# Optimization experiments

Hardware: AMD Instinct MI355X
Metric: run time of the kernel (lower is better)

Reference implementation:

```python
import jax, jax.numpy as jnp
import numpy as np
from jax import lax

B, DIM, H, W = 4, 128, 256, 256
SD, FD, GD = DIM // 2, DIM // 4, DIM // 4
EPS = 1e-6


def conv1x1(x, w):
    # w: (O, I), x: (B, I, H, W)
    return jnp.einsum('oi,bihw->bohw', w, x)


def dwconv3(x, w):
    # depthwise 3x3, w: (C, 1, 3, 3)
    return lax.conv_general_dilated(
        x, w, window_strides=(1, 1), padding='SAME',
        feature_group_count=x.shape[1],
        dimension_numbers=('NCHW', 'OIHW', 'NCHW'))


def rmsnorm(x, scale):
    rms = jnp.sqrt(jnp.mean(x * x, axis=1, keepdims=True) + EPS)
    return x / rms * scale[None, :, None, None]


def setup_inputs() -> dict:
    key = jax.random.key(0)
    ks = jax.random.split(key, 12)
    s = 0.02
    return {
        'x': jax.random.normal(ks[0], (B, DIM, H, W), jnp.float32),
        'norm1_scale': jnp.ones((DIM,), jnp.float32),
        'wq': jax.random.normal(ks[1], (SD, SD), jnp.float32) * s,
        'wk': jax.random.normal(ks[2], (SD, SD), jnp.float32) * s,
        'wv': jax.random.normal(ks[3], (SD, SD), jnp.float32) * s,
        'dwqk': jax.random.normal(ks[4], (SD, 1, 3, 3), jnp.float32) * s,
        'rel_bias': jnp.zeros((SD, 1, 1), jnp.float32),
        'spatial_scale': jnp.full((1,), SD ** (-0.5), jnp.float32),
        'cweight': jax.random.normal(ks[5], (FD, 1, 1, 2), jnp.float32) * s,
        'fnorm_scale': jnp.ones((FD,), jnp.float32),
        'freq_w': jax.random.normal(ks[6], (FD, FD), jnp.float32) * s,
        'gate_w': jax.random.normal(ks[7], (GD, GD), jnp.float32) * s,
        'proj_out_w': jax.random.normal(ks[8], (DIM, DIM), jnp.float32) * s,
        'norm2_scale': jnp.ones((DIM,), jnp.float32),
        'mlp_w1': jax.random.normal(ks[9], (2 * DIM, DIM), jnp.float32) * s,
        'mlp_w2': jax.random.normal(ks[10], (DIM, 2 * DIM), jnp.float32) * s,
        'mlp_dw': jax.random.normal(ks[11], (DIM, 1, 3, 3), jnp.float32) * s,
    }


def reference(x, norm1_scale, wq, wk, wv, dwqk, rel_bias, spatial_scale,
              cweight, fnorm_scale, freq_w, gate_w, proj_out_w, norm2_scale,
              mlp_w1, mlp_w2, mlp_dw):
    residual = x
    xn = rmsnorm(x, norm1_scale)
    xs, xf, xg = xn[:, :SD], xn[:, SD:SD + FD], xn[:, SD + FD:]

    # ---- spatial branch: linear attention with global kv pooling ----
    q = dwconv3(conv1x1(xs, wq), dwqk)
    k = dwconv3(conv1x1(xs, wk), dwqk)
    v = conv1x1(xs, wv)
    q = jax.nn.elu(q) + 1.0
    k = jax.nn.elu(k) + 1.0
    kv = jnp.sum(k * v, axis=(2, 3), keepdims=True)          # (B,SD,1,1)
    denom = jnp.sum(k, axis=(2, 3), keepdims=True) + 1e-6    # (B,SD,1,1)
    xs_out = q * kv / denom + v
    xs_out = xs_out * (spatial_scale + rel_bias)[None]       # (1,SD,1,1) bcast

    # ---- frequency branch: learnable FFT filter ----
    xff = jnp.fft.rfft2(xf, norm='ortho')                    # (B,FD,H,W//2+1)
    wc = cweight[..., 0] + 1j * cweight[..., 1]              # (FD,1,1) complex
    xff = xff * wc
    xf_sp = jnp.fft.irfft2(xff, s=(H, W), norm='ortho')
    xf_out = conv1x1(rmsnorm(xf_sp, fnorm_scale), freq_w)

    # ---- gate branch ----
    g = jax.nn.sigmoid(conv1x1(xg, gate_w))                  # (B,GD,H,W)

    combined = jnp.concatenate([xs_out, xf_out], axis=1)     # (B,3*GD,H,W)
    gate_b = jnp.tile(g, (1, combined.shape[1] // GD, 1, 1))
    combined = combined * gate_b
    combined = jnp.concatenate([combined, g], axis=1)        # (B,DIM,H,W)
    combined = conv1x1(combined, proj_out_w)
    combined = rmsnorm(combined, norm2_scale)

    # ---- conv MLP ----
    h = conv1x1(combined, mlp_w1)
    h = jax.nn.gelu(h, approximate=False)
    h = conv1x1(h, mlp_w2)
    h = dwconv3(h, mlp_dw)
    return h + residual
```

## Files before the change

### kernel.cpp

```cpp
#include <hip/hip_runtime.h>
#include <hip/hip_bf16.h>
#include <math.h>

#define B_    4
#define CDIM  128
#define Hh    256
#define Ww    256
#define SD_   64
#define FD_   32
#define HW    (Hh*Ww)
#define NPOS  (B_*HW)

typedef __hip_bfloat16 bf16;
typedef __attribute__((ext_vector_type(8))) short short8;
typedef __attribute__((ext_vector_type(4))) float f32x4;

__device__ __forceinline__ bf16 f2b(float f){ return __float2bfloat16(f); }
__device__ __forceinline__ float b2f(bf16 h){ return __bfloat162float(h); }
__device__ __forceinline__ unsigned short f2us(float f){
  __hip_bfloat16 h=__float2bfloat16(f);
  return *reinterpret_cast<unsigned short*>(&h);
}
__device__ __forceinline__ float us2f(unsigned short u){
  unsigned int i=((unsigned int)u)<<16;
  return __uint_as_float(i);
}

__global__ __launch_bounds__(256) void k_prep(const float* __restrict__ projw,
   const float* __restrict__ w1, const float* __restrict__ w2,
   const float* __restrict__ wq, const float* __restrict__ wk, const float* __restrict__ wv,
   bf16* __restrict__ pw_f, bf16* __restrict__ w1_f, bf16* __restrict__ w2_f,
   bf16* __restrict__ wq_f, bf16* __restrict__ wk_f, bf16* __restrict__ wv_f)
{
  int idx=blockIdx.x*256+threadIdx.x;
  if(idx>=94208) return;
  const float* src; bf16* dst; int NKS,K,rel;
  if(idx<16384){ src=projw; dst=pw_f; NKS=4; K=128; rel=idx; }
  else if(idx<49152){ src=w1; dst=w1_f; NKS=4; K=128; rel=idx-16384; }
  else if(idx<81920){ src=w2; dst=w2_f; NKS=8; K=256; rel=idx-49152; }
  else if(idx<86016){ src=wq; dst=wq_f; NKS=2; K=64; rel=idx-81920; }
  else if(idx<90112){ src=wk; dst=wk_f; NKS=2; K=64; rel=idx-86016; }
  else { src=wv; dst=wv_f; NKS=2; K=64; rel=idx-90112; }
  int e=rel&7, lane=(rel>>3)&63, rest=rel>>9;
  int ks=rest%NKS, cb=rest/NKS;
  int row=cb*16+(lane&15);
  int k=ks*32+(lane>>4)*8+e;
  dst[rel]=f2b(src[row*K+k]);
}

__global__ __launch_bounds__(256) void k_invr(const float* __restrict__ x, float* __restrict__ invr){
  const int p=blockIdx.x*256+threadIdx.x;
  const int b=p/HW, rem=p-b*HW;
  const float* xp=x+(size_t)b*CDIM*HW+rem;
  float s=0.f;
  #pragma unroll 4
  for(int c=0;c<CDIM;c++){ float v=xp[(size_t)c*HW]; s+=v*v; }
  invr[p]=rsqrtf(s*(1.f/CDIM)+1e-6f);
}

__global__ __launch_bounds__(256) void k_qkv(const float* __restrict__ x, const float* __restrict__ invr,
    const float* __restrict__ n1s, const bf16* __restrict__ wq_f, const bf16* __restrict__ wk_f,
    const bf16* __restrict__ wv_f,
    bf16* __restrict__ qpre, bf16* __restrict__ kpre, bf16* __restrict__ vout)
{
  __shared__ __align__(16) char smem[8192];
  const int t=threadIdx.x;
  const int p0=blockIdx.x*64;
  const int b=p0/HW, rem0=p0-b*HW;
  for(int i=t;i<4096;i+=256){
    int ci=i>>6, p=i&63;
    float v_=x[(size_t)(b*CDIM+ci)*HW+rem0+p]*invr[p0+p]*n1s[ci];
    *(unsigned short*)(smem + (p<<7) + ((ci*2) ^ ((p&7)<<4))) = f2us(v_);
  }
  __syncthreads();
  const int l=t&63, w=t>>6;
  const int ploc=w*16+(l&15);
  const int lg=l>>4;
  const int psw=(ploc&7)<<4;
  short8 bfr[2];
  #pragma unroll
  for(int ks=0;ks<2;ks++){
    bfr[ks]=*(const short8*)(smem + (ploc<<7) + ((ks*64+lg*16) ^ psw));
  }
  const int pg=rem0+ploc;
  #pragma unroll
  for(int cb=0;cb<4;cb++){
    f32x4 aq={0.f,0.f,0.f,0.f}, ak={0.f,0.f,0.f,0.f}, av={0.f,0.f,0.f,0.f};
    #pragma unroll
    for(int ks=0;ks<2;ks++){
      short8 afq=*(const short8*)(wq_f + (size_t)((cb*2+ks)*64+l)*8);
      short8 afk=*(const short8*)(wk_f + (size_t)((cb*2+ks)*64+l)*8);
      short8 afv=*(const short8*)(wv_f + (size_t)((cb*2+ks)*64+l)*8);
      aq=__builtin_amdgcn_mfma_f32_16x16x32_bf16(afq,bfr[ks],aq,0,0,0);
      ak=__builtin_amdgcn_mfma_f32_16x16x32_bf16(afk,bfr[ks],ak,0,0,0);
      av=__builtin_amdgcn_mfma_f32_16x16x32_bf16(afv,bfr[ks],av,0,0,0);
    }
    int c0=cb*16+lg*4;
    #pragma unroll
    for(int j=0;j<4;j++){
      size_t off=(size_t)(b*SD_+c0+j)*HW+pg;
      qpre[off]=f2b(aq[j]); kpre[off]=f2b(ak[j]); vout[off]=f2b(av[j]);
    }
  }
}

__global__ __launch_bounds__(256) void k_spatial(const bf16* __restrict__ qpre, const bf16* __restrict__ kpre,
  const bf16* __restrict__ vin, const float* __restrict__ dwqk,
  bf16* __restrict__ qout, float* __restrict__ kvsum, float* __restrict__ densum)
{
  const int blk=blockIdx.x;
  const int tile=blk&7, bc=blk>>3, c=bc&63;
  const int h0=tile*32;
  const int t=threadIdx.x;
  __shared__ unsigned short qs[34*256];
  __shared__ unsigned short ks_[34*256];
  __shared__ float pkv[4], pk[4];
  const size_t base=(size_t)bc*HW;
  for(int i=t;i<34*32;i+=256){
    int r=i>>5, c8=(i&31)<<3;
    int hr=h0+r-1;
    short8 zq={0,0,0,0,0,0,0,0}, zk={0,0,0,0,0,0,0,0};
    if(hr>=0&&hr<Hh){
      zq=*(const short8*)(qpre+base+(size_t)hr*Ww+c8);
      zk=*(const short8*)(kpre+base+(size_t)hr*Ww+c8);
    }
    *(short8*)(qs+r*256+c8)=zq;
    *(short8*)(ks_+r*256+c8)=zk;
  }
  __syncthreads();
  const float* dwc=dwqk+c*9;
  float d[9];
  #pragma unroll
  for(int j=0;j<9;j++) d[j]=dwc[j];
  float qw[3][3], kw[3][3];
  #pragma unroll
  for(int r=0;r<2;r++){
    qw[r][0]=(t>0)?us2f(qs[r*256+t-1]):0.f;
    qw[r][1]=us2f(qs[r*256+t]);
    qw[r][2]=(t<255)?us2f(qs[r*256+t+1]):0.f;
    kw[r][0]=(t>0)?us2f(ks_[r*256+t-1]):0.f;
    kw[r][1]=us2f(ks_[r*256+t]);
    kw[r][2]=(t<255)?us2f(ks_[r*256+t+1]):0.f;
  }
  float s1=0.f,s2=0.f;
  #pragma unroll
  for(int i=0;i<32;i++){
    const int rn=i+2, sn=(i+2)%3, sA=(i+1)%3, s0=i%3;
    qw[sn][0]=(t>0)?us2f(qs[rn*256+t-1]):0.f;
    qw[sn][1]=us2f(qs[rn*256+t]);
    qw[sn][2]=(t<255)?us2f(qs[rn*256+t+1]):0.f;
    kw[sn][0]=(t>0)?us2f(ks_[rn*256+t-1]):0.f;
    kw[sn][1]=us2f(ks_[rn*256+t]);
    kw[sn][2]=(t<255)?us2f(ks_[rn*256+t+1]):0.f;
    float qa=qw[s0][0]*d[0]+qw[s0][1]*d[1]+qw[s0][2]*d[2]
            +qw[sA][0]*d[3]+qw[sA][1]*d[4]+qw[sA][2]*d[5]
            +qw[sn][0]*d[6]+qw[sn][1]*d[7]+qw[sn][2]*d[8];
    float ka=kw[s0][0]*d[0]+kw[s0][1]*d[1]+kw[s0][2]*d[2]
            +kw[sA][0]*d[3]+kw[sA][1]*d[4]+kw[sA][2]*d[5]
            +kw[sn][0]*d[6]+kw[sn][1]*d[7]+kw[sn][2]*d[8];
    float qq=qa>0.f?qa+1.f:expf(qa);
    float kk=ka>0.f?ka+1.f:expf(ka);
    size_t o=base+(size_t)(h0+i)*Ww+t;
    qout[o]=f2b(qq);
    float vv=b2f(vin[o]);
    s1+=kk*vv; s2+=kk;
  }
  #pragma unroll
  for(int off=32;off>0;off>>=1){ s1+=__shfl_down(s1,off,64); s2+=__shfl_down(s2,off,64); }
  const int wid=t>>6, lane=t&63;
  if(lane==0){ pkv[wid]=s1; pk[wid]=s2; }
  __syncthreads();
  if(t==0){
    atomicAdd(&kvsum[bc], pkv[0]+pkv[1]+pkv[2]+pkv[3]);
    atomicAdd(&densum[bc], pk[0]+pk[1]+pk[2]+pk[3]);
  }
}

__global__ __launch_bounds__(256) void k_hil(const float* __restrict__ x, const float* __restrict__ invr,
  const float* __restrict__ n1s, const float* __restrict__ cw, bf16* __restrict__ xfsp)
{
  const int blk=blockIdx.x;
  const int h=blk&255, bcf=blk>>8, cf=bcf&31, b=bcf>>5;
  const int t=threadIdx.x;
  __shared__ float xr[256];
  __shared__ float tap[128];
  const int c=SD_+cf;
  const size_t rowx=(size_t)(b*CDIM+c)*HW+(size_t)h*Ww;
  const size_t rowp=(size_t)b*HW+(size_t)h*Ww;
  xr[t]=x[rowx+t]*invr[rowp+t]*n1s[c];
  if(t<128){
    int d=2*t+1;
    float dd = (d<128)? (float)d : (float)(256-d);
    float sg = (d<128)? -1.f : 1.f;
    float a=dd*(float)(3.14159265358979323846/256.0);
    tap[t]=sg*(1.f/128.f)*(cosf(a)/sinf(a));
  }
  __syncthreads();
  float acc=0.f;
  #pragma unroll 8
  for(int j=0;j<128;j++){
    acc+=tap[j]*xr[(t-(2*j+1))&255];
  }
  float a_=cw[2*cf], b_=cw[2*cf+1];
  xfsp[(size_t)(b*FD_+cf)*HW+(size_t)h*Ww+t]=f2b(a_*xr[t]+b_*acc);
}

__global__ __launch_bounds__(256) void k_main(
  const float* __restrict__ x, const float* __restrict__ invr, const float* __restrict__ n1s,
  const bf16* __restrict__ q, const bf16* __restrict__ v, const bf16* __restrict__ xfsp,
  const float* __restrict__ kvsum, const float* __restrict__ densum,
  const float* __restrict__ relb, const float* __restrict__ sscale,
  const float* __restrict__ fnorm, const float* __restrict__ freq_w, const float* __restrict__ gate_w,
  const bf16* __restrict__ pw_f, const float* __restrict__ n2s,
  const bf16* __restrict__ w1_f, const bf16* __restrict__ w2_f,
  bf16* __restrict__ h2)
{
  __shared__ __align__(16) char smem[49152];
  float* xg  =(float*)(smem+16384);
  float* invp=(float*)(smem+24576);
  float* xfs =(float*)(smem+32768);
  float* gsh =(float*)(smem+40960);

  const int t=threadIdx.x;
  const int p0=blockIdx.x*64;
  const int b=p0/HW;
  const int rem0=p0-b*HW;

  for(int i=t;i<2048;i+=256){
    int ci=i>>6,p=i&63;
    xfs[i]=b2f(xfsp[(size_t)(b*FD_+ci)*HW+rem0+p]);
    xg[i] =x[(size_t)(b*CDIM+96+ci)*HW+rem0+p]*invr[p0+p]*n1s[96+ci];
  }
  __syncthreads();
  if(t<64){
    float s=0.f;
    #pragma unroll
    for(int ci=0;ci<32;ci++){ float vv=xfs[ci*64+t]; s+=vv*vv; }
    invp[t]=rsqrtf(s*(1.f/32.f)+1e-6f);
  }
  for(int i=t;i<2048;i+=256){
    int co=i>>6,p=i&63;
    int cou=__builtin_amdgcn_readfirstlane(co);
    float acc=0.f;
    #pragma unroll
    for(int ci=0;ci<32;ci+=4){
      float4 w4=*(const float4*)(gate_w+cou*32+ci);
      acc+=w4.x*xg[ci*64+p]+w4.y*xg[(ci+1)*64+p]+w4.z*xg[(ci+2)*64+p]+w4.w*xg[(ci+3)*64+p];
    }
    gsh[i]=1.f/(1.f+expf(-acc));
  }
  __syncthreads();
  for(int i=t;i<2048;i+=256){
    int ci=i>>6,p=i&63;
    xfs[i]*=invp[p]*fnorm[ci];
  }
  __syncthreads();
  const float ss=sscale[0];
  for(int i=t;i<8192;i+=256){
    int c=i>>6,p=i&63;
    float g=gsh[(c&31)*64+p];
    float val;
    if(c<64){
      size_t off=(size_t)(b*SD_+c)*HW+rem0+p;
      float kvv=kvsum[b*SD_+c];
      float dd=densum[b*SD_+c]+1e-6f;
      val=(b2f(q[off])*kvv/dd + b2f(v[off]))*(ss+relb[c]);
    } else if(c<96){
      int cou=__builtin_amdgcn_readfirstlane(c-64);
      float acc=0.f;
      #pragma unroll
      for(int ci=0;ci<32;ci+=4){
        float4 w4=*(const float4*)(freq_w+cou*32+ci);
        acc+=w4.x*xfs[ci*64+p]+w4.y*xfs[(ci+1)*64+p]+w4.z*xfs[(ci+2)*64+p]+w4.w*xfs[(ci+3)*64+p];
      }
      val=acc;
    } else {
      val=1.f;
    }
    *(unsigned short*)(smem + ((p<<8) + ((c*2) ^ ((p&7)<<4)))) = f2us(val*g);
  }
  __syncthreads();
  const int l=t&63, w=t>>6;
  const int ploc=w*16+(l&15);
  const int lg=l>>4;
  const int psw=(ploc&7)<<4;

  short8 bf[4];
  #pragma unroll
  for(int ks=0;ks<4;ks++){
    int kb=ks*64+lg*16;
    bf[ks]=*(const short8*)(smem + ((ploc<<8) + (kb ^ psw)));
  }
  f32x4 acc[8];
  #pragma unroll
  for(int cb=0;cb<8;cb++){
    f32x4 a={0.f,0.f,0.f,0.f};
    #pragma unroll
    for(int ks=0;ks<4;ks++){
      short8 af=*(const short8*)(pw_f + (size_t)((cb*4+ks)*64+l)*8);
      a=__builtin_amdgcn_mfma_f32_16x16x32_bf16(af,bf[ks],a,0,0,0);
    }
    acc[cb]=a;
  }
  float s2=0.f;
  #pragma unroll
  for(int cb=0;cb<8;cb++){
    s2+=acc[cb][0]*acc[cb][0]+acc[cb][1]*acc[cb][1]+acc[cb][2]*acc[cb][2]+acc[cb][3]*acc[cb][3];
  }
  s2+=__shfl_xor(s2,16);
  s2+=__shfl_xor(s2,32);
  float inv2=rsqrtf(s2*(1.f/128.f)+1e-6f);
  #pragma unroll
  for(int cb=0;cb<8;cb++){
    int c0=cb*16+lg*4;
    float4 nv=*(const float4*)(n2s+c0);
    float v0=acc[cb][0]*inv2*nv.x, v1=acc[cb][1]*inv2*nv.y;
    float v2=acc[cb][2]*inv2*nv.z, v3=acc[cb][3]*inv2*nv.w;
    unsigned u01=(unsigned)f2us(v0) | (((unsigned)f2us(v1))<<16);
    unsigned u23=(unsigned)f2us(v2) | (((unsigned)f2us(v3))<<16);
    int base=(ploc<<8) + ((c0*2) ^ psw);
    *(unsigned*)(smem+base)=u01;
    *(unsigned*)(smem+base+4)=u23;
  }
  #pragma unroll
  for(int ks=0;ks<4;ks++){
    int kb=ks*64+lg*16;
    bf[ks]=*(const short8*)(smem + ((ploc<<8) + (kb ^ psw)));
  }
  #pragma unroll
  for(int half=0;half<2;half++){
    f32x4 hacc[8];
    #pragma unroll
    for(int cb=0;cb<8;cb++){
      f32x4 a={0.f,0.f,0.f,0.f};
      #pragma unroll
      for(int ks=0;ks<4;ks++){
        short8 af=*(const short8*)(w1_f + (size_t)(((half*8+cb)*4+ks)*64+l)*8);
        a=__builtin_amdgcn_mfma_f32_16x16x32_bf16(af,bf[ks],a,0,0,0);
      }
      hacc[cb]=a;
    }
    #pragma unroll
    for(int cb=0;cb<8;cb++){
      int c0=(half*8+cb)*16+lg*4;
      float g0=hacc[cb][0], g1=hacc[cb][1], g2=hacc[cb][2], g3=hacc[cb][3];
      g0=0.5f*g0*(1.f+erff(g0*0.70710678118654752f));
      g1=0.5f*g1*(1.f+erff(g1*0.70710678118654752f));
      g2=0.5f*g2*(1.f+erff(g2*0.70710678118654752f));
      g3=0.5f*g3*(1.f+erff(g3*0.70710678118654752f));
      unsigned u01=(unsigned)f2us(g0) | (((unsigned)f2us(g1))<<16);
      unsigned u23=(unsigned)f2us(g2) | (((unsigned)f2us(g3))<<16);
      int base=16384 + (ploc<<9) + ((c0*2) ^ psw);
      *(unsigned*)(smem+base)=u01;
      *(unsigned*)(smem+base+4)=u23;
    }
  }
  short8 bf2[8];
  #pragma unroll
  for(int ks=0;ks<8;ks++){
    int kb=ks*64+lg*16;
    bf2[ks]=*(const short8*)(smem + (16384 + (ploc<<9) + (kb ^ psw)));
  }
  const int pg=rem0+ploc;
  #pragma unroll
  for(int cb=0;cb<8;cb++){
    f32x4 a={0.f,0.f,0.f,0.f};
    #pragma unroll
    for(int ks=0;ks<8;ks++){
      short8 af=*(const short8*)(w2_f + (size_t)((cb*8+ks)*64+l)*8);
      a=__builtin_amdgcn_mfma_f32_16x16x32_bf16(af,bf2[ks],a,0,0,0);
    }
    int c0=cb*16+lg*4;
    h2[(size_t)(b*CDIM+c0  )*HW+pg]=f2b(a[0]);
    h2[(size_t)(b*CDIM+c0+1)*HW+pg]=f2b(a[1]);
    h2[(size_t)(b*CDIM+c0+2)*HW+pg]=f2b(a[2]);
    h2[(size_t)(b*CDIM+c0+3)*HW+pg]=f2b(a[3]);
  }
}

__global__ __launch_bounds__(256) void k_final(const bf16* __restrict__ h2, const float* __restrict__ x,
  const float* __restrict__ mdw, float* __restrict__ out)
{
  const int blk=blockIdx.x;
  const int tile=blk&7, bc=blk>>3, c=bc&127;
  const int h0=tile*32;
  const int t=threadIdx.x;
  __shared__ unsigned short hs[34*256];
  const size_t base=(size_t)bc*HW;
  for(int i=t;i<34*32;i+=256){
    int r=i>>5, c8=(i&31)<<3;
    int hr=h0+r-1;
    short8 z={0,0,0,0,0,0,0,0};
    if(hr>=0&&hr<Hh) z=*(const short8*)(h2+base+(size_t)hr*Ww+c8);
    *(short8*)(hs+r*256+c8)=z;
  }
  __syncthreads();
  const float* dwc=mdw+c*9;
  float d[9];
  #pragma unroll
  for(int j=0;j<9;j++) d[j]=dwc[j];
  float w_[3][3];
  #pragma unroll
  for(int r=0;r<2;r++){
    w_[r][0]=(t>0)?us2f(hs[r*256+t-1]):0.f;
    w_[r][1]=us2f(hs[r*256+t]);
    w_[r][2]=(t<255)?us2f(hs[r*256+t+1]):0.f;
  }
  #pragma unroll
  for(int i=0;i<32;i++){
    const int rn=i+2, sn=(i+2)%3, sA=(i+1)%3, s0=i%3;
    w_[sn][0]=(t>0)?us2f(hs[rn*256+t-1]):0.f;
    w_[sn][1]=us2f(hs[rn*256+t]);
    w_[sn][2]=(t<255)?us2f(hs[rn*256+t+1]):0.f;
    float acc=w_[s0][0]*d[0]+w_[s0][1]*d[1]+w_[s0][2]*d[2]
             +w_[sA][0]*d[3]+w_[sA][1]*d[4]+w_[sA][2]*d[5]
             +w_[sn][0]*d[6]+w_[sn][1]*d[7]+w_[sn][2]*d[8];
    size_t o=base+(size_t)(h0+i)*Ww+t;
    out[o]=acc+x[o];
  }
}

static const size_t O_INVR = 0;
static const size_t O_V    = (size_t)1<<20;
static const size_t O_Q    = O_V    + (size_t)33554432;
static const size_t O_QPRE = O_Q    + (size_t)33554432;
static const size_t O_KPRE = O_QPRE + (size_t)33554432;
static const size_t O_XFSP = O_KPRE + (size_t)33554432;
static const size_t O_KV   = O_XFSP + (size_t)16777216;
static const size_t O_DEN  = O_KV   + 4096;
static const size_t O_PWF  = O_KV   + 8192;
static const size_t O_W1F  = O_PWF  + 32768;
static const size_t O_W2F  = O_W1F  + 65536;
static const size_t O_WQF  = O_W2F  + 65536;
static const size_t O_WKF  = O_WQF  + 8192;
static const size_t O_WVF  = O_WKF  + 8192;
static const size_t O_H2   = O_QPRE;

extern "C" void kernel_launch(void* const* d_in, const int* in_sizes, int n_in,
                              void* d_out, int out_size, void* d_ws, size_t ws_size,
                              hipStream_t stream)
{
  const float* x     =(const float*)d_in[0];
  const float* n1s   =(const float*)d_in[1];
  const float* wq    =(const float*)d_in[2];
  const float* wk    =(const float*)d_in[3];
  const float* wv    =(const float*)d_in[4];
  const float* dwqk  =(const float*)d_in[5];
  const float* relb  =(const float*)d_in[6];
  const float* sscale=(const float*)d_in[7];
  const float* cw    =(const float*)d_in[8];
  const float* fnorm =(const float*)d_in[9];
  const float* freq_w=(const float*)d_in[10];
  const float* gate_w=(const float*)d_in[11];
  const float* projw =(const float*)d_in[12];
  const float* n2s   =(const float*)d_in[13];
  const float* w1    =(const float*)d_in[14];
  const float* w2    =(const float*)d_in[15];
  const float* mdw   =(const float*)d_in[16];

  char* ws=(char*)d_ws;
  float* invr =(float*)(ws+O_INVR);
  bf16* v    =(bf16*)(ws+O_V);
  bf16* q    =(bf16*)(ws+O_Q);
  bf16* qpre =(bf16*)(ws+O_QPRE);
  bf16* kpre =(bf16*)(ws+O_KPRE);
  bf16* xfsp =(bf16*)(ws+O_XFSP);
  float* kvsum=(float*)(ws+O_KV);
  float* densum=(float*)(ws+O_DEN);
  bf16* pw_f =(bf16*)(ws+O_PWF);
  bf16* w1_f =(bf16*)(ws+O_W1F);
  bf16* w2_f =(bf16*)(ws+O_W2F);
  bf16* wq_f =(bf16*)(ws+O_WQF);
  bf16* wk_f =(bf16*)(ws+O_WKF);
  bf16* wv_f =(bf16*)(ws+O_WVF);
  bf16* h2   =(bf16*)(ws+O_H2);
  float* out =(float*)d_out;

  k_prep<<<dim3(368),dim3(256),0,stream>>>(projw,w1,w2,wq,wk,wv,pw_f,w1_f,w2_f,wq_f,wk_f,wv_f);
  k_invr<<<dim3(NPOS/256),dim3(256),0,stream>>>(x,invr);
  k_qkv<<<dim3(NPOS/64),dim3(256),0,stream>>>(x,invr,n1s,wq_f,wk_f,wv_f,qpre,kpre,v);
  hipMemsetAsync(ws+O_KV,0,8192,stream);
  k_spatial<<<dim3(B_*SD_*8),dim3(256),0,stream>>>(qpre,kpre,v,dwqk,q,kvsum,densum);
  k_hil<<<dim3(B_*FD_*Hh),dim3(256),0,stream>>>(x,invr,n1s,cw,xfsp);
  k_main<<<dim3(NPOS/64),dim3(256),0,stream>>>(x,invr,n1s,q,v,xfsp,kvsum,densum,
                                               relb,sscale,fnorm,freq_w,gate_w,pw_f,n2s,w1_f,w2_f,h2);
  k_final<<<dim3(B_*CDIM*8),dim3(256),0,stream>>>(h2,x,mdw,out);
}
```

Before: 765.2 us.

## Fuse RMS stats into qkv, MFMA gate/freq convs, tanh GELU, streamed MLP

Folds the standalone inverse-RMS kernel into k_qkv, which now reads x once, computes the per-pixel RMS and writes invr for later kernels. In k_main the gate and frequency 1x1 convs move from scalar FP32 loops to bf16 MFMA using prepacked weights, and the MLP's second GEMM is interleaved with the first per half to cut LDS use. Exact erf GELU becomes a tanh approximation, expf becomes __expf, and k_hil processes 8 rows per block. These lower memory traffic, launch count and ALU work, at the cost of extra bf16 rounding and approximation error in GELU and the gate/frequency convs.

```diff
diff --git a/kernel.cpp b/kernel.cpp
--- a/kernel.cpp
+++ b/kernel.cpp
@@ -25,22 +25,32 @@
   unsigned int i=((unsigned int)u)<<16;
   return __uint_as_float(i);
 }
+__device__ __forceinline__ float gelu_t(float x){
+  float u=0.7978845608f*(x+0.044715f*x*x*x);
+  float e=__expf(2.f*u);
+  float th=1.f-2.f/(e+1.f);
+  return 0.5f*x*(1.f+th);
+}
 
 __global__ __launch_bounds__(256) void k_prep(const float* __restrict__ projw,
    const float* __restrict__ w1, const float* __restrict__ w2,
    const float* __restrict__ wq, const float* __restrict__ wk, const float* __restrict__ wv,
+   const float* __restrict__ gatew, const float* __restrict__ freqw,
    bf16* __restrict__ pw_f, bf16* __restrict__ w1_f, bf16* __restrict__ w2_f,
-   bf16* __restrict__ wq_f, bf16* __restrict__ wk_f, bf16* __restrict__ wv_f)
+   bf16* __restrict__ wq_f, bf16* __restrict__ wk_f, bf16* __restrict__ wv_f,
+   bf16* __restrict__ gw_f, bf16* __restrict__ fw_f)
 {
   int idx=blockIdx.x*256+threadIdx.x;
-  if(idx>=94208) return;
+  if(idx>=96256) return;
   const float* src; bf16* dst; int NKS,K,rel;
   if(idx<16384){ src=projw; dst=pw_f; NKS=4; K=128; rel=idx; }
   else if(idx<49152){ src=w1; dst=w1_f; NKS=4; K=128; rel=idx-16384; }
   else if(idx<81920){ src=w2; dst=w2_f; NKS=8; K=256; rel=idx-49152; }
   else if(idx<86016){ src=wq; dst=wq_f; NKS=2; K=64; rel=idx-81920; }
   else if(idx<90112){ src=wk; dst=wk_f; NKS=2; K=64; rel=idx-86016; }
-  else { src=wv; dst=wv_f; NKS=2; K=64; rel=idx-90112; }
+  else if(idx<94208){ src=wv; dst=wv_f; NKS=2; K=64; rel=idx-90112; }
+  else if(idx<95232){ src=gatew; dst=gw_f; NKS=1; K=32; rel=idx-94208; }
+  else { src=freqw; dst=fw_f; NKS=1; K=32; rel=idx-95232; }
   int e=rel&7, lane=(rel>>3)&63, rest=rel>>9;
   int ks=rest%NKS, cb=rest/NKS;
   int row=cb*16+(lane&15);
@@ -48,29 +58,41 @@
   dst[rel]=f2b(src[row*K+k]);
 }
 
-__global__ __launch_bounds__(256) void k_invr(const float* __restrict__ x, float* __restrict__ invr){
-  const int p=blockIdx.x*256+threadIdx.x;
-  const int b=p/HW, rem=p-b*HW;
-  const float* xp=x+(size_t)b*CDIM*HW+rem;
-  float s=0.f;
-  #pragma unroll 4
-  for(int c=0;c<CDIM;c++){ float v=xp[(size_t)c*HW]; s+=v*v; }
-  invr[p]=rsqrtf(s*(1.f/CDIM)+1e-6f);
-}
-
-__global__ __launch_bounds__(256) void k_qkv(const float* __restrict__ x, const float* __restrict__ invr,
+__global__ __launch_bounds__(256) void k_qkv(const float* __restrict__ x,
     const float* __restrict__ n1s, const bf16* __restrict__ wq_f, const bf16* __restrict__ wk_f,
     const bf16* __restrict__ wv_f,
-    bf16* __restrict__ qpre, bf16* __restrict__ kpre, bf16* __restrict__ vout)
-{
-  __shared__ __align__(16) char smem[8192];
+    bf16* __restrict__ qpre, bf16* __restrict__ kpre, bf16* __restrict__ vout,
+    float* __restrict__ invr)
+{
+  __shared__ float sqp[256];
+  __shared__ float invl[64];
+  __shared__ __align__(16) char qb[8192];
   const int t=threadIdx.x;
   const int p0=blockIdx.x*64;
   const int b=p0/HW, rem0=p0-b*HW;
-  for(int i=t;i<4096;i+=256){
-    int ci=i>>6, p=i&63;
-    float v_=x[(size_t)(b*CDIM+ci)*HW+rem0+p]*invr[p0+p]*n1s[ci];
-    *(unsigned short*)(smem + (p<<7) + ((ci*2) ^ ((p&7)<<4))) = f2us(v_);
+  const int p=t&63, g=t>>6;
+  float xv[32];
+  {
+    float ss=0.f;
+    const float* xbase = x + (size_t)(b*CDIM+g*32)*HW + rem0 + p;
+    #pragma unroll
+    for(int k=0;k<32;k++){ float v_=xbase[(size_t)k*HW]; xv[k]=v_; ss+=v_*v_; }
+    sqp[t]=ss;
+  }
+  __syncthreads();
+  if(t<64){
+    float s=sqp[t]+sqp[64+t]+sqp[128+t]+sqp[192+t];
+    float iv=rsqrtf(s*(1.f/128.f)+1e-6f);
+    invl[t]=iv; invr[p0+t]=iv;
+  }
+  __syncthreads();
+  if(g<2){
+    float iv=invl[p];
+    #pragma unroll
+    for(int k=0;k<32;k++){
+      int ci=g*32+k;
+      *(unsigned short*)(qb + (p<<7) + ((ci*2) ^ ((p&7)<<4))) = f2us(xv[k]*iv*n1s[ci]);
+    }
   }
   __syncthreads();
   const int l=t&63, w=t>>6;
@@ -80,7 +102,7 @@
   short8 bfr[2];
   #pragma unroll
   for(int ks=0;ks<2;ks++){
-    bfr[ks]=*(const short8*)(smem + (ploc<<7) + ((ks*64+lg*16) ^ psw));
+    bfr[ks]=*(const short8*)(qb + (ploc<<7) + ((ks*64+lg*16) ^ psw));
   }
   const int pg=rem0+ploc;
   #pragma unroll
@@ -158,8 +180,8 @@
     float ka=kw[s0][0]*d[0]+kw[s0][1]*d[1]+kw[s0][2]*d[2]
             +kw[sA][0]*d[3]+kw[sA][1]*d[4]+kw[sA][2]*d[5]
             +kw[sn][0]*d[6]+kw[sn][1]*d[7]+kw[sn][2]*d[8];
-    float qq=qa>0.f?qa+1.f:expf(qa);
-    float kk=ka>0.f?ka+1.f:expf(ka);
+    float qq=qa>0.f?qa+1.f:__expf(qa);
+    float kk=ka>0.f?ka+1.f:__expf(ka);
     size_t o=base+(size_t)(h0+i)*Ww+t;
     qout[o]=f2b(qq);
     float vv=b2f(vin[o]);
@@ -180,14 +202,20 @@
   const float* __restrict__ n1s, const float* __restrict__ cw, bf16* __restrict__ xfsp)
 {
   const int blk=blockIdx.x;
-  const int h=blk&255, bcf=blk>>8, cf=bcf&31, b=bcf>>5;
+  const int tile=blk&31, bcf=blk>>5, cf=bcf&31, b=bcf>>5;
+  const int h0=tile*8;
   const int t=threadIdx.x;
-  __shared__ float xr[256];
+  __shared__ float xr[8*256];
   __shared__ float tap[128];
   const int c=SD_+cf;
-  const size_t rowx=(size_t)(b*CDIM+c)*HW+(size_t)h*Ww;
-  const size_t rowp=(size_t)b*HW+(size_t)h*Ww;
-  xr[t]=x[rowx+t]*invr[rowp+t]*n1s[c];
+  const size_t rowx=(size_t)(b*CDIM+c)*HW+(size_t)h0*Ww;
+  const size_t rowp=(size_t)b*HW+(size_t)h0*Ww;
+  const float nsc=n1s[c];
+  #pragma unroll
+  for(int k=0;k<8;k++){
+    int i=t+k*256;
+    xr[i]=x[rowx+i]*invr[rowp+i]*nsc;
+  }
   if(t<128){
     int d=2*t+1;
     float dd = (d<128)? (float)d : (float)(256-d);
@@ -196,13 +224,16 @@
     tap[t]=sg*(1.f/128.f)*(cosf(a)/sinf(a));
   }
   __syncthreads();
-  float acc=0.f;
-  #pragma unroll 8
-  for(int j=0;j<128;j++){
-    acc+=tap[j]*xr[(t-(2*j+1))&255];
-  }
   float a_=cw[2*cf], b_=cw[2*cf+1];
-  xfsp[(size_t)(b*FD_+cf)*HW+(size_t)h*Ww+t]=f2b(a_*xr[t]+b_*acc);
+  #pragma unroll
+  for(int r=0;r<8;r++){
+    float acc=0.f;
+    #pragma unroll 8
+    for(int j=0;j<128;j++){
+      acc+=tap[j]*xr[r*256 + ((t-(2*j+1))&255)];
+    }
+    xfsp[(size_t)(b*FD_+cf)*HW+(size_t)(h0+r)*Ww+t]=f2b(a_*xr[r*256+t]+b_*acc);
+  }
 }
 
 __global__ __launch_bounds__(256) void k_main(
@@ -210,86 +241,111 @@
   const bf16* __restrict__ q, const bf16* __restrict__ v, const bf16* __restrict__ xfsp,
   const float* __restrict__ kvsum, const float* __restrict__ densum,
   const float* __restrict__ relb, const float* __restrict__ sscale,
-  const float* __restrict__ fnorm, const float* __restrict__ freq_w, const float* __restrict__ gate_w,
+  const float* __restrict__ fnorm, const bf16* __restrict__ fw_f, const bf16* __restrict__ gw_f,
   const bf16* __restrict__ pw_f, const float* __restrict__ n2s,
   const bf16* __restrict__ w1_f, const bf16* __restrict__ w2_f,
   bf16* __restrict__ h2)
 {
-  __shared__ __align__(16) char smem[49152];
-  float* xg  =(float*)(smem+16384);
-  float* invp=(float*)(smem+24576);
-  float* xfs =(float*)(smem+32768);
-  float* gsh =(float*)(smem+40960);
+  __shared__ __align__(16) char smem[32768];
+  float* sqp =(float*)(smem+16384);
+  float* invp=(float*)(smem+17408);
 
   const int t=threadIdx.x;
   const int p0=blockIdx.x*64;
   const int b=p0/HW;
   const int rem0=p0-b*HW;
-
-  for(int i=t;i<2048;i+=256){
-    int ci=i>>6,p=i&63;
-    xfs[i]=b2f(xfsp[(size_t)(b*FD_+ci)*HW+rem0+p]);
-    xg[i] =x[(size_t)(b*CDIM+96+ci)*HW+rem0+p]*invr[p0+p]*n1s[96+ci];
+  const int l=t&63, w=t>>6;
+  const int ploc=w*16+(l&15);
+  const int lg=l>>4;
+  const int psw=(ploc&7)<<4;
+
+  float xv[8];
+  {
+    const int p=t&63, g=t>>6;
+    float ss=0.f;
+    #pragma unroll
+    for(int k=0;k<8;k++){
+      int ci=g*8+k;
+      float v_=b2f(xfsp[(size_t)(b*FD_+ci)*HW+rem0+p]);
+      xv[k]=v_; ss+=v_*v_;
+    }
+    sqp[t]=ss;
+    float iv=invr[p0+p];
+    #pragma unroll
+    for(int k=0;k<8;k++){
+      int ci=g*8+k;
+      float gv=x[(size_t)(b*CDIM+96+ci)*HW+rem0+p]*iv*n1s[96+ci];
+      *(unsigned short*)(smem + 18432 + (p<<6) + ((ci*2) ^ ((p&3)<<4))) = f2us(gv);
+    }
   }
   __syncthreads();
   if(t<64){
-    float s=0.f;
-    #pragma unroll
-    for(int ci=0;ci<32;ci++){ float vv=xfs[ci*64+t]; s+=vv*vv; }
+    float s=sqp[t]+sqp[64+t]+sqp[128+t]+sqp[192+t];
     invp[t]=rsqrtf(s*(1.f/32.f)+1e-6f);
   }
-  for(int i=t;i<2048;i+=256){
-    int co=i>>6,p=i&63;
-    int cou=__builtin_amdgcn_readfirstlane(co);
-    float acc=0.f;
-    #pragma unroll
-    for(int ci=0;ci<32;ci+=4){
-      float4 w4=*(const float4*)(gate_w+cou*32+ci);
-      acc+=w4.x*xg[ci*64+p]+w4.y*xg[(ci+1)*64+p]+w4.z*xg[(ci+2)*64+p]+w4.w*xg[(ci+3)*64+p];
-    }
-    gsh[i]=1.f/(1.f+expf(-acc));
-  }
-  __syncthreads();
-  for(int i=t;i<2048;i+=256){
-    int ci=i>>6,p=i&63;
-    xfs[i]*=invp[p]*fnorm[ci];
-  }
-  __syncthreads();
+  {
+    short8 bg=*(const short8*)(smem + 18432 + (ploc<<6) + ((lg*16) ^ ((ploc&3)<<4)));
+    #pragma unroll
+    for(int cb=0;cb<2;cb++){
+      short8 ag=*(const short8*)(gw_f + (size_t)(cb*64+l)*8);
+      f32x4 a={0.f,0.f,0.f,0.f};
+      a=__builtin_amdgcn_mfma_f32_16x16x32_bf16(ag,bg,a,0,0,0);
+      #pragma unroll
+      for(int j=0;j<4;j++){
+        int cch=cb*16+lg*4+j;
+        float gj=1.f/(1.f+__expf(-a[j]));
+        *(unsigned short*)(smem + 26624 + cch*128 + ploc*2) = f2us(gj);
+      }
+    }
+  }
+  __syncthreads();
+  {
+    const int p=t&63, g=t>>6;
+    float iv=invp[p];
+    #pragma unroll
+    for(int k=0;k<8;k++){
+      int ci=g*8+k;
+      *(unsigned short*)(smem + 22528 + (p<<6) + ((ci*2) ^ ((p&3)<<4))) = f2us(xv[k]*iv*fnorm[ci]);
+    }
+  }
+  __syncthreads();
+  {
+    short8 bff=*(const short8*)(smem + 22528 + (ploc<<6) + ((lg*16) ^ ((ploc&3)<<4)));
+    #pragma unroll
+    for(int cb=0;cb<2;cb++){
+      short8 af=*(const short8*)(fw_f + (size_t)(cb*64+l)*8);
+      f32x4 a={0.f,0.f,0.f,0.f};
+      a=__builtin_amdgcn_mfma_f32_16x16x32_bf16(af,bff,a,0,0,0);
+      #pragma unroll
+      for(int j=0;j<4;j++){
+        int cf=cb*16+lg*4+j;
+        float gj=us2f(*(const unsigned short*)(smem + 26624 + cf*128 + ploc*2));
+        int c=64+cf;
+        *(unsigned short*)(smem + (ploc<<8) + ((c*2) ^ psw)) = f2us(a[j]*gj);
+      }
+    }
+  }
   const float ss=sscale[0];
-  for(int i=t;i<8192;i+=256){
-    int c=i>>6,p=i&63;
-    float g=gsh[(c&31)*64+p];
+  for(int i=t;i<6144;i+=256){
+    int cc=i>>6, p=i&63;
+    int c=(cc<64)? cc : cc+32;
+    float g=us2f(*(const unsigned short*)(smem + 26624 + (c&31)*128 + p*2));
     float val;
     if(c<64){
       size_t off=(size_t)(b*SD_+c)*HW+rem0+p;
       float kvv=kvsum[b*SD_+c];
       float dd=densum[b*SD_+c]+1e-6f;
       val=(b2f(q[off])*kvv/dd + b2f(v[off]))*(ss+relb[c]);
-    } else if(c<96){
-      int cou=__builtin_amdgcn_readfirstlane(c-64);
-      float acc=0.f;
-      #pragma unroll
-      for(int ci=0;ci<32;ci+=4){
-        float4 w4=*(const float4*)(freq_w+cou*32+ci);
-        acc+=w4.x*xfs[ci*64+p]+w4.y*xfs[(ci+1)*64+p]+w4.z*xfs[(ci+2)*64+p]+w4.w*xfs[(ci+3)*64+p];
-      }
-      val=acc;
     } else {
       val=1.f;
     }
-    *(unsigned short*)(smem + ((p<<8) + ((c*2) ^ ((p&7)<<4)))) = f2us(val*g);
-  }
-  __syncthreads();
-  const int l=t&63, w=t>>6;
-  const int ploc=w*16+(l&15);
-  const int lg=l>>4;
-  const int psw=(ploc&7)<<4;
-
+    *(unsigned short*)(smem + (p<<8) + ((c*2) ^ ((p&7)<<4))) = f2us(val*g);
+  }
+  __syncthreads();
   short8 bf[4];
   #pragma unroll
   for(int ks=0;ks<4;ks++){
-    int kb=ks*64+lg*16;
-    bf[ks]=*(const short8*)(smem + ((ploc<<8) + (kb ^ psw)));
+    bf[ks]=*(const short8*)(smem + (ploc<<8) + (((ks*64+lg*16)) ^ psw));
   }
   f32x4 acc[8];
   #pragma unroll
@@ -324,12 +380,13 @@
   }
   #pragma unroll
   for(int ks=0;ks<4;ks++){
-    int kb=ks*64+lg*16;
-    bf[ks]=*(const short8*)(smem + ((ploc<<8) + (kb ^ psw)));
-  }
+    bf[ks]=*(const short8*)(smem + (ploc<<8) + (((ks*64+lg*16)) ^ psw));
+  }
+  f32x4 acc2[8];
+  #pragma unroll
+  for(int cb=0;cb<8;cb++){ acc2[cb]=(f32x4){0.f,0.f,0.f,0.f}; }
   #pragma unroll
   for(int half=0;half<2;half++){
-    f32x4 hacc[8];
     #pragma unroll
     for(int cb=0;cb<8;cb++){
       f32x4 a={0.f,0.f,0.f,0.f};
@@ -338,43 +395,32 @@
         short8 af=*(const short8*)(w1_f + (size_t)(((half*8+cb)*4+ks)*64+l)*8);
         a=__builtin_amdgcn_mfma_f32_16x16x32_bf16(af,bf[ks],a,0,0,0);
       }
-      hacc[cb]=a;
-    }
-    #pragma unroll
-    for(int cb=0;cb<8;cb++){
-      int c0=(half*8+cb)*16+lg*4;
-      float g0=hacc[cb][0], g1=hacc[cb][1], g2=hacc[cb][2], g3=hacc[cb][3];
-      g0=0.5f*g0*(1.f+erff(g0*0.70710678118654752f));
-      g1=0.5f*g1*(1.f+erff(g1*0.70710678118654752f));
-      g2=0.5f*g2*(1.f+erff(g2*0.70710678118654752f));
-      g3=0.5f*g3*(1.f+erff(g3*0.70710678118654752f));
+      int c0=cb*16+lg*4;
+      float g0=gelu_t(a[0]), g1=gelu_t(a[1]), g2=gelu_t(a[2]), g3=gelu_t(a[3]);
       unsigned u01=(unsigned)f2us(g0) | (((unsigned)f2us(g1))<<16);
       unsigned u23=(unsigned)f2us(g2) | (((unsigned)f2us(g3))<<16);
-      int base=16384 + (ploc<<9) + ((c0*2) ^ psw);
+      int base=16384 + (ploc<<8) + ((c0*2) ^ psw);
       *(unsigned*)(smem+base)=u01;
       *(unsigned*)(smem+base+4)=u23;
     }
-  }
-  short8 bf2[8];
-  #pragma unroll
-  for(int ks=0;ks<8;ks++){
-    int kb=ks*64+lg*16;
-    bf2[ks]=*(const short8*)(smem + (16384 + (ploc<<9) + (kb ^ psw)));
+    #pragma unroll
+    for(int ks=0;ks<4;ks++){
+      short8 bh=*(const short8*)(smem + 16384 + (ploc<<8) + (((ks*64+lg*16)) ^ psw));
+      #pragma unroll
+      for(int cb=0;cb<8;cb++){
+        short8 af=*(const short8*)(w2_f + (size_t)((cb*8+half*4+ks)*64+l)*8);
+        acc2[cb]=__builtin_amdgcn_mfma_f32_16x16x32_bf16(af,bh,acc2[cb],0,0,0);
+      }
+    }
   }
   const int pg=rem0+ploc;
   #pragma unroll
   for(int cb=0;cb<8;cb++){
-    f32x4 a={0.f,0.f,0.f,0.f};
-    #pragma unroll
-    for(int ks=0;ks<8;ks++){
-      short8 af=*(const short8*)(w2_f + (size_t)((cb*8+ks)*64+l)*8);
-      a=__builtin_amdgcn_mfma_f32_16x16x32_bf16(af,bf2[ks],a,0,0,0);
-    }
     int c0=cb*16+lg*4;
-    h2[(size_t)(b*CDIM+c0  )*HW+pg]=f2b(a[0]);
-    h2[(size_t)(b*CDIM+c0+1)*HW+pg]=f2b(a[1]);
-    h2[(size_t)(b*CDIM+c0+2)*HW+pg]=f2b(a[2]);
-    h2[(size_t)(b*CDIM+c0+3)*HW+pg]=f2b(a[3]);
+    h2[(size_t)(b*CDIM+c0  )*HW+pg]=f2b(acc2[cb][0]);
+    h2[(size_t)(b*CDIM+c0+1)*HW+pg]=f2b(acc2[cb][1]);
+    h2[(size_t)(b*CDIM+c0+2)*HW+pg]=f2b(acc2[cb][2]);
+    h2[(size_t)(b*CDIM+c0+3)*HW+pg]=f2b(acc2[cb][3]);
   }
 }
 
@@ -434,6 +480,8 @@
 static const size_t O_WQF  = O_W2F  + 65536;
 static const size_t O_WKF  = O_WQF  + 8192;
 static const size_t O_WVF  = O_WKF  + 8192;
+static const size_t O_GWF  = O_WVF  + 8192;
+static const size_t O_FWF  = O_GWF  + 2048;
 static const size_t O_H2   = O_QPRE;
 
 extern "C" void kernel_launch(void* const* d_in, const int* in_sizes, int n_in,
@@ -473,16 +521,18 @@
   bf16* wq_f =(bf16*)(ws+O_WQF);
   bf16* wk_f =(bf16*)(ws+O_WKF);
   bf16* wv_f =(bf16*)(ws+O_WVF);
+  bf16* gw_f =(bf16*)(ws+O_GWF);
+  bf16* fw_f =(bf16*)(ws+O_FWF);
   bf16* h2   =(bf16*)(ws+O_H2);
   float* out =(float*)d_out;
 
-  k_prep<<<dim3(368),dim3(256),0,stream>>>(projw,w1,w2,wq,wk,wv,pw_f,w1_f,w2_f,wq_f,wk_f,wv_f);
-  k_invr<<<dim3(NPOS/256),dim3(256),0,stream>>>(x,invr);
-  k_qkv<<<dim3(NPOS/64),dim3(256),0,stream>>>(x,invr,n1s,wq_f,wk_f,wv_f,qpre,kpre,v);
+  k_prep<<<dim3(376),dim3(256),0,stream>>>(projw,w1,w2,wq,wk,wv,gate_w,freq_w,
+                                           pw_f,w1_f,w2_f,wq_f,wk_f,wv_f,gw_f,fw_f);
+  k_qkv<<<dim3(NPOS/64),dim3(256),0,stream>>>(x,n1s,wq_f,wk_f,wv_f,qpre,kpre,v,invr);
   hipMemsetAsync(ws+O_KV,0,8192,stream);
   k_spatial<<<dim3(B_*SD_*8),dim3(256),0,stream>>>(qpre,kpre,v,dwqk,q,kvsum,densum);
-  k_hil<<<dim3(B_*FD_*Hh),dim3(256),0,stream>>>(x,invr,n1s,cw,xfsp);
+  k_hil<<<dim3(B_*FD_*32),dim3(256),0,stream>>>(x,invr,n1s,cw,xfsp);
   k_main<<<dim3(NPOS/64),dim3(256),0,stream>>>(x,invr,n1s,q,v,xfsp,kvsum,densum,
-                                               relb,sscale,fnorm,freq_w,gate_w,pw_f,n2s,w1_f,w2_f,h2);
+                                               relb,sscale,fnorm,fw_f,gw_f,pw_f,n2s,w1_f,w2_f,h2);
   k_final<<<dim3(B_*CDIM*8),dim3(256),0,stream>>>(h2,x,mdw,out);
 }
```

Result: faster. 655.8 us (-14.3%).
